# Performance work log

Measured on AMD Instinct MI355X. Metric: run time of the kernel, lower is better.

Reference implementation:

```python
import jax, jax.numpy as jnp
import numpy as np

MUL0, MUL1 = 128, 64
DIM1 = MUL0 + 3 * MUL1          # 320 = dim of 128x0e + 64x1o
DIM2 = 4                        # 1x0e + 1x1o
WDIM, H = 16, 64
# per-instruction weight sizes (mul_in2 = 1), e3nn instruction order
N1 = MUL0 * MUL0                # (0e x 0e -> 0e)
N2 = MUL0 * MUL1                # (0e x 1o -> 1o)
N3 = MUL1 * MUL1                # (1o x 0e -> 1o)
N4 = MUL1 * MUL0                # (1o x 1o -> 0e)
WNUMEL = N1 + N2 + N3 + N4      # 36864
FAN = MUL0 + MUL1               # summed fan-in per output slice = 192
PW0 = float(np.sqrt(1.0 / FAN))         # path weight, component/element norm, l_out=0
PW1 = float(np.sqrt(3.0 / FAN))         # l_out=1 (alpha = 2l+1 = 3)
INV_SQRT3 = float(1.0 / np.sqrt(3.0))   # wigner_3j(1,1,0)/(0,1,1)/(1,0,1) entries
SQRT_K = float(1.0 / np.sqrt(FAN))      # tp_rescale correction (output divided by this)


def setup_inputs() -> dict:
    key = jax.random.key(0)
    ks = jax.random.split(key, 8)
    N = 4096

    def lin(k, fin, fout):
        k1, k2 = jax.random.split(k)
        lim = 1.0 / np.sqrt(fin)
        W = jax.random.uniform(k1, (fin, fout), minval=-lim, maxval=lim, dtype=jnp.float32)
        b = jax.random.uniform(k2, (fout,), minval=-lim, maxval=lim, dtype=jnp.float32)
        return W, b

    W0, b0 = lin(ks[3], WDIM, H)
    W1, b1 = lin(ks[4], H, H)
    W2, b2 = lin(ks[5], H, WNUMEL)
    return {
        "data_in1": jax.random.normal(ks[0], (N, DIM1), dtype=jnp.float32),
        "data_in2": jax.random.normal(ks[1], (N, DIM2), dtype=jnp.float32),
        "weight": jax.random.normal(ks[2], (N, WDIM), dtype=jnp.float32),
        "W0": W0, "b0": b0, "W1": W1, "b1": b1, "W2": W2, "b2": b2,
        "bias": jax.random.uniform(ks[6], (MUL0,), minval=-SQRT_K, maxval=SQRT_K, dtype=jnp.float32),
    }


def _forward(data_in1, data_in2, weight, W0, b0, W1, b1, W2, b2, bias):
    # weight-generating MLP: 16 -> 64 -> 64 -> weight_numel
    h = jax.nn.relu(weight @ W0 + b0)
    h = jax.nn.relu(h @ W1 + b1)
    w = h @ W2 + b2                                   # [N, WNUMEL] per-sample tp weights
    # split inputs into irrep blocks
    s1 = data_in1[:, :MUL0]                           # [N,128]  128x0e
    v1 = data_in1[:, MUL0:].reshape(-1, MUL1, 3)      # [N,64,3]  64x1o
    s2 = data_in2[:, 0]                               # [N]       1x0e
    v2 = data_in2[:, 1:4]                             # [N,3]     1x1o
    # per-instruction weight views (uvw with v=1 collapsed)
    Wa = w[:, :N1].reshape(-1, MUL0, MUL0)                   # 0e x 0e -> 0e
    Wb = w[:, N1:N1 + N2].reshape(-1, MUL0, MUL1)            # 0e x 1o -> 1o
    Wc = w[:, N1 + N2:N1 + N2 + N3].reshape(-1, MUL1, MUL1)  # 1o x 0e -> 1o
    Wd = w[:, N1 + N2 + N3:].reshape(-1, MUL1, MUL0)         # 1o x 1o -> 0e
    dot12 = jnp.einsum('eui,ei->eu', v1, v2)          # [N,64]
    # scalar (0e) output slice: paths Wa (w3j=1) and Wd (w3j = delta/sqrt(3))
    out0 = PW0 * (jnp.einsum('euw,eu->ew', Wa, s1) * s2[:, None]
                  + INV_SQRT3 * jnp.einsum('euw,eu->ew', Wd, dot12))
    # vector (1o) output slice: paths Wb and Wc (w3j = delta/sqrt(3))
    out1 = PW1 * INV_SQRT3 * (
        jnp.einsum('euw,eu->ew', Wb, s1)[:, :, None] * v2[:, None, :]
        + jnp.einsum('euw,eui->ewi', Wc, v1) * s2[:, None, None])
    out = jnp.concatenate([out0, out1.reshape(-1, 3 * MUL1)], axis=1)  # [N,320]
    out = out / SQRT_K                                # tp_rescale: divide by sqrt_k correction
    out = out.at[:, :MUL0].add(bias)                  # bias added on 0e slice only
    return out


def reference(data_in1, data_in2, weight, W0, b0, W1, b1, W2, b2, bias):
    return _forward(data_in1, data_in2, weight, W0, b0, W1, b1, W2, b2, bias)
```

## Files before the change

kernel.cpp:

```cpp
#include <hip/hip_runtime.h>
#include <hip/hip_bf16.h>

typedef __attribute__((ext_vector_type(8))) short short8;
typedef __attribute__((ext_vector_type(4))) float f32x4;

constexpr int N1 = 16384, N2 = 8192, N3 = 4096;
constexpr int WN = 36864;
constexpr float ISQ3 = 0.57735026918962576451f;

__device__ __forceinline__ unsigned short f2bf(float f) {
  unsigned u = __builtin_bit_cast(unsigned, f);
  u += 0x7fffu + ((u >> 16) & 1u);
  return (unsigned short)(u >> 16);
}

#define MFMA(a, b, c) __builtin_amdgcn_mfma_f32_16x16x32_bf16((a), (b), (c), 0, 0, 0)

__global__ __launch_bounds__(256)
void k_prep(const float* __restrict__ wgt, const float* __restrict__ W0,
            const float* __restrict__ b0, const float* __restrict__ W1,
            const float* __restrict__ b1, const float* __restrict__ W2,
            const float* __restrict__ b2, const float* __restrict__ bias,
            const float* __restrict__ d1, const float* __restrict__ d2,
            float* __restrict__ H, unsigned short* __restrict__ Bp,
            float* __restrict__ sAg, float* __restrict__ sBg,
            float* __restrict__ sDg, float* __restrict__ sCg,
            float* __restrict__ d2T, float* __restrict__ out) {
  __shared__ __align__(16) float shm[10400];
  const int bid = blockIdx.x;
  const int tid = threadIdx.x;

  if (bid < 512) {
    float* s1s = shm;
    float* v1s = shm + 1024;
    float* dts = shm + 2560;
    float* s2s = shm + 3072;
    float* v2s = shm + 3080;
    const int e0 = bid * 8;
    for (int x = tid; x < 8 * 320; x += 256) {
      int e = x / 320, c = x % 320;
      float v = d1[(size_t)(e0 + e) * 320 + c];
      if (c < 128) s1s[e * 128 + c] = v;
      else { int q = c - 128; v1s[(e * 64 + q / 3) * 3 + q % 3] = v; }
    }
    if (tid < 32) {
      int e = tid >> 2, c = tid & 3;
      float v = d2[(size_t)(e0 + e) * 4 + c];
      if (c == 0) s2s[e] = v; else v2s[e * 3 + c - 1] = v;
    }
    __syncthreads();
    for (int x = tid; x < 8 * 64; x += 256) {
      int e = x >> 6, u = x & 63;
      dts[e * 64 + u] = v1s[(e * 64 + u) * 3] * v2s[e * 3] +
                        v1s[(e * 64 + u) * 3 + 1] * v2s[e * 3 + 1] +
                        v1s[(e * 64 + u) * 3 + 2] * v2s[e * 3 + 2];
    }
    __syncthreads();
    for (int c = tid; c < 320; c += 256) {
      if (c < 128) {
        const int w = c;
        float ta[8] = {0,0,0,0,0,0,0,0}, td[8] = {0,0,0,0,0,0,0,0};
        for (int u = 0; u < 128; ++u) {
          float bv = b2[u * 128 + w];
#pragma unroll
          for (int e = 0; e < 8; ++e) ta[e] = fmaf(s1s[e * 128 + u], bv, ta[e]);
        }
        for (int u = 0; u < 64; ++u) {
          float bv = b2[N1 + N2 + N3 + u * 128 + w];
#pragma unroll
          for (int e = 0; e < 8; ++e) td[e] = fmaf(dts[e * 64 + u], bv, td[e]);
        }
        const float bw = bias[w];
#pragma unroll
        for (int e = 0; e < 8; ++e)
          out[(size_t)(e0 + e) * 320 + c] = fmaf(s2s[e], ta[e], ISQ3 * td[e]) + bw;
      } else {
        const int q = c - 128, w = q / 3, i = q % 3;
        float tb[8] = {0,0,0,0,0,0,0,0}, tc[8] = {0,0,0,0,0,0,0,0};
        for (int u = 0; u < 128; ++u) {
          float bv = b2[N1 + u * 64 + w];
#pragma unroll
          for (int e = 0; e < 8; ++e) tb[e] = fmaf(s1s[e * 128 + u], bv, tb[e]);
        }
        for (int u = 0; u < 64; ++u) {
          float bv = b2[N1 + N2 + u * 64 + w];
#pragma unroll
          for (int e = 0; e < 8; ++e) tc[e] = fmaf(v1s[(e * 64 + u) * 3 + i], bv, tc[e]);
        }
#pragma unroll
        for (int e = 0; e < 8; ++e)
          out[(size_t)(e0 + e) * 320 + c] = tb[e] * v2s[e * 3 + i] + tc[e] * s2s[e];
      }
    }
  } else if (bid < 1664) {
    const int g = (bid - 512) * 256 + tid;
    const int lane = g & 63;
    const int nth = g >> 6;
    const int kh = nth & 1, nt = nth >> 1;
    const int n = nt * 16 + (lane & 15);
    const int k0 = kh * 32 + (lane >> 4) * 8;
    short8 v;
#pragma unroll
    for (int q = 0; q < 8; ++q) v[q] = (short)f2bf(W2[(size_t)(k0 + q) * WN + n]);
    *(short8*)(Bp + (size_t)g * 8) = v;
  } else if (bid < 2688) {
    float* h0s = shm;
    const int r = tid >> 6, jj = tid & 63;
    const int e = (bid - 1664) * 4 + r;
    float a = b0[jj];
#pragma unroll
    for (int i = 0; i < 16; ++i) a = fmaf(wgt[e * 16 + i], W0[i * 64 + jj], a);
    h0s[r * 64 + jj] = fmaxf(a, 0.f);
    __syncthreads();
    float a1 = b1[jj];
#pragma unroll
    for (int i = 0; i < 64; ++i) a1 = fmaf(h0s[r * 64 + i], W1[i * 64 + jj], a1);
    H[e * 64 + jj] = fmaxf(a1, 0.f);
  } else {
    float* d1s = shm;
    float* d2s = shm + 10272;
    const int e0 = (bid - 2688) * 32;
    for (int x = tid; x < 32 * 320; x += 256) {
      int e = x / 320, c = x % 320;
      d1s[e * 321 + c] = d1[(size_t)(e0 + e) * 320 + c];
    }
    if (tid < 128) d2s[tid] = d2[(size_t)e0 * 4 + tid];
    __syncthreads();
    const int e = tid & 31;
    const float s2 = d2s[e * 4 + 0];
    const float w1 = d2s[e * 4 + 1], w2 = d2s[e * 4 + 2], w3 = d2s[e * 4 + 3];
    for (int row = (tid >> 5); row < 516; row += 8) {
      float v; float* dst;
      if (row < 128)      { v = d1s[e * 321 + row] * s2;            dst = sAg + (size_t)row * 4096; }
      else if (row < 256) { v = d1s[e * 321 + (row - 128)];         dst = sBg + (size_t)(row - 128) * 4096; }
      else if (row < 320) { int u = row - 256;
        v = ISQ3 * (d1s[e * 321 + 128 + 3 * u] * w1 + d1s[e * 321 + 129 + 3 * u] * w2 +
                    d1s[e * 321 + 130 + 3 * u] * w3);               dst = sDg + (size_t)u * 4096; }
      else if (row < 512) { v = d1s[e * 321 + 128 + (row - 320)] * s2; dst = sCg + (size_t)(row - 320) * 4096; }
      else                { v = d2s[e * 4 + (row - 512)];           dst = d2T + (size_t)(row - 512) * 4096; }
      dst[e0 + e] = v;
    }
  }
}

__global__ __launch_bounds__(256, 3)
void k_main(const float* __restrict__ sAg, const float* __restrict__ sBg,
            const float* __restrict__ sDg, const float* __restrict__ sCg,
            const float* __restrict__ d2T, const float* __restrict__ H,
            const unsigned short* __restrict__ Bp, float* __restrict__ out) {
  __shared__ __align__(16) float lds[8704];
  const int bid = blockIdx.x, tid = threadIdx.x;
  const int wid = tid >> 6, lane = tid & 63;
  const int nl = lane & 15, grp = lane >> 4;
  const short8* Bp8 = (const short8*)Bp;
  const f32x4 Z = {0.f, 0.f, 0.f, 0.f};

  if (bid < 512) {
    const int j = bid & 7, tile = bid >> 3, e0 = tile * 64;
    short8 h00, h01, h10, h11, h20, h21, h30, h31;
    {
      const float* hp; short8 v0, v1;
#define LOADH(EF, N0, N1_)                                                     \
      hp = H + (size_t)(e0 + 16 * EF + nl) * 64 + grp * 8;                     \
      _Pragma("unroll") for (int q = 0; q < 8; ++q) {                          \
        v0[q] = (short)f2bf(hp[q]); v1[q] = (short)f2bf(hp[32 + q]); }         \
      N0 = v0; N1_ = v1;
      LOADH(0, h00, h01) LOADH(1, h10, h11) LOADH(2, h20, h21) LOADH(3, h30, h31)
#undef LOADH
    }
    const int uA0 = wid * 32, uD0 = wid * 16;
    const short8* pA = Bp8 + (size_t)(uA0 * 8 + j) * 128 + lane;
    const short8* pD = Bp8 + (size_t)(1792 + uD0 * 8 + j) * 128 + lane;
    const float* qA0 = sAg + (size_t)uA0 * 4096 + e0 + nl;
    const float* qA1 = qA0 + 4096;
    const float* qD  = sDg + (size_t)uD0 * 4096 + e0 + nl;

    short8 A00 = pA[0], A01 = pA[64], A10 = pA[1024], A11 = pA[1088]; pA += 2048;
    short8 D00 = pD[0], D01 = pD[64]; pD += 1024;
    float sa0 = qA0[0], sa1 = qA0[16], sa2 = qA0[32], sa3 = qA0[48];
    float sa4 = qA1[0], sa5 = qA1[16], sa6 = qA1[32], sa7 = qA1[48]; qA0 += 8192; qA1 += 8192;
    float sd0 = qD[0], sd1 = qD[16], sd2 = qD[32], sd3 = qD[48]; qD += 4096;
    short8 B00 = pA[0], B01 = pA[64], B10 = pA[1024], B11 = pA[1088]; pA += 2048;
    short8 E00 = pD[0], E01 = pD[64]; pD += 1024;
    float ta0 = qA0[0], ta1 = qA0[16], ta2 = qA0[32], ta3 = qA0[48];
    float ta4 = qA1[0], ta5 = qA1[16], ta6 = qA1[32], ta7 = qA1[48]; qA0 += 8192; qA1 += 8192;
    float td0 = qD[0], td1 = qD[16], td2 = qD[32], td3 = qD[48]; qD += 4096;

    f32x4 accA[4] = {Z, Z, Z, Z};
    f32x4 accD[4] = {Z, Z, Z, Z};

#define QUAD(P0, P1, S0, S1, S2, S3, AC) do { f32x4 t_;                        \
    t_ = Z; t_ = MFMA(P0, h00, t_); t_ = MFMA(P1, h01, t_); AC[0] += (S0) * t_; \
    t_ = Z; t_ = MFMA(P0, h10, t_); t_ = MFMA(P1, h11, t_); AC[1] += (S1) * t_; \
    t_ = Z; t_ = MFMA(P0, h20, t_); t_ = MFMA(P1, h21, t_); AC[2] += (S2) * t_; \
    t_ = Z; t_ = MFMA(P0, h30, t_); t_ = MFMA(P1, h31, t_); AC[3] += (S3) * t_; } while (0)

#pragma unroll
    for (int t = 0; t < 16; t += 2) {
      QUAD(A00, A01, sa0, sa1, sa2, sa3, accA);
      QUAD(A10, A11, sa4, sa5, sa6, sa7, accA);
      QUAD(D00, D01, sd0, sd1, sd2, sd3, accD);
      if (t < 14) {
        A00 = pA[0]; A01 = pA[64]; A10 = pA[1024]; A11 = pA[1088]; pA += 2048;
        D00 = pD[0]; D01 = pD[64]; pD += 1024;
        sa0 = qA0[0]; sa1 = qA0[16]; sa2 = qA0[32]; sa3 = qA0[48];
        sa4 = qA1[0]; sa5 = qA1[16]; sa6 = qA1[32]; sa7 = qA1[48]; qA0 += 8192; qA1 += 8192;
        sd0 = qD[0]; sd1 = qD[16]; sd2 = qD[32]; sd3 = qD[48]; qD += 4096;
      }
      QUAD(B00, B01, ta0, ta1, ta2, ta3, accA);
      QUAD(B10, B11, ta4, ta5, ta6, ta7, accA);
      QUAD(E00, E01, td0, td1, td2, td3, accD);
      if (t < 13) {
        B00 = pA[0]; B01 = pA[64]; B10 = pA[1024]; B11 = pA[1088]; pA += 2048;
        E00 = pD[0]; E01 = pD[64]; pD += 1024;
        ta0 = qA0[0]; ta1 = qA0[16]; ta2 = qA0[32]; ta3 = qA0[48];
        ta4 = qA1[0]; ta5 = qA1[16]; ta6 = qA1[32]; ta7 = qA1[48]; qA0 += 8192; qA1 += 8192;
        td0 = qD[0]; td1 = qD[16]; td2 = qD[32]; td3 = qD[48]; qD += 4096;
      }
    }
#undef QUAD

#pragma unroll
    for (int eF = 0; eF < 4; ++eF) {
      f32x4 fin = accA[eF] + accD[eF];
      *(f32x4*)&lds[wid * 1280 + (16 * eF + nl) * 20 + grp * 4] = fin;
    }
    __syncthreads();
    {
      const int e = tid >> 2, w4 = (tid & 3) * 4;
      f32x4 s = Z;
#pragma unroll
      for (int wv = 0; wv < 4; ++wv) s += *(const f32x4*)&lds[wv * 1280 + e * 20 + w4];
      f32x4* op = (f32x4*)(out + (size_t)(e0 + e) * 320 + j * 16 + w4);
      *op = *op + s;
    }
  } else {
    const int idx = bid - 512;
    const int j = idx & 3;
    const int tile = ((idx >> 3) << 1) + ((idx >> 2) & 1);
    const int e0 = tile * 32;
    short8 h00, h01, h10, h11;
    {
      const float* hp; short8 v0, v1;
#define LOADH(EF, N0, N1_)                                                     \
      hp = H + (size_t)(e0 + 16 * EF + nl) * 64 + grp * 8;                     \
      _Pragma("unroll") for (int q = 0; q < 8; ++q) {                          \
        v0[q] = (short)f2bf(hp[q]); v1[q] = (short)f2bf(hp[32 + q]); }         \
      N0 = v0; N1_ = v1;
      LOADH(0, h00, h01) LOADH(1, h10, h11)
#undef LOADH
    }
    const int uB0 = wid * 32, uC0 = wid * 16;
    const short8* pB = Bp8 + (size_t)(1024 + uB0 * 4 + j) * 128 + lane;
    const short8* pC = Bp8 + (size_t)(1536 + uC0 * 4 + j) * 128 + lane;
    const float* qB0 = sBg + (size_t)uB0 * 4096 + e0 + nl;
    const float* qB1 = qB0 + 4096;
    const float* qC0 = sCg + (size_t)(uC0 * 3) * 4096 + e0 + nl;
    const float* qC1 = qC0 + 4096;
    const float* qC2 = qC0 + 8192;

    short8 A00 = pB[0], A01 = pB[64], A10 = pB[512], A11 = pB[576]; pB += 1024;
    short8 C00 = pC[0], C01 = pC[64]; pC += 512;
    float sb0 = qB0[0], sb1 = qB0[16], sb2 = qB1[0], sb3 = qB1[16]; qB0 += 8192; qB1 += 8192;
    float sc00 = qC0[0], sc01 = qC0[16], sc10 = qC1[0], sc11 = qC1[16],
          sc20 = qC2[0], sc21 = qC2[16]; qC0 += 12288; qC1 += 12288; qC2 += 12288;
    short8 B00 = pB[0], B01 = pB[64], B10 = pB[512], B11 = pB[576]; pB += 1024;
    short8 E00 = pC[0], E01 = pC[64]; pC += 512;
    float tb0 = qB0[0], tb1 = qB0[16], tb2 = qB1[0], tb3 = qB1[16]; qB0 += 8192; qB1 += 8192;
    float tc00 = qC0[0], tc01 = qC0[16], tc10 = qC1[0], tc11 = qC1[16],
          tc20 = qC2[0], tc21 = qC2[16]; qC0 += 12288; qC1 += 12288; qC2 += 12288;

    f32x4 accB[2] = {Z, Z};
    f32x4 accC0[2] = {Z, Z}, accC1[2] = {Z, Z}, accC2[2] = {Z, Z};

#define DUO(P0, P1, S0, S1) do { f32x4 t_;                                     \
    t_ = Z; t_ = MFMA(P0, h00, t_); t_ = MFMA(P1, h01, t_); accB[0] += (S0) * t_; \
    t_ = Z; t_ = MFMA(P0, h10, t_); t_ = MFMA(P1, h11, t_); accB[1] += (S1) * t_; } while (0)
#define CTRIO(P0, P1, X00, X01, X10, X11, X20, X21) do { f32x4 u0_, u1_;       \
    u0_ = Z; u0_ = MFMA(P0, h00, u0_); u0_ = MFMA(P1, h01, u0_);               \
    u1_ = Z; u1_ = MFMA(P0, h10, u1_); u1_ = MFMA(P1, h11, u1_);               \
    accC0[0] += (X00) * u0_; accC0[1] += (X01) * u1_;                          \
    accC1[0] += (X10) * u0_; accC1[1] += (X11) * u1_;                          \
    accC2[0] += (X20) * u0_; accC2[1] += (X21) * u1_; } while (0)

#pragma unroll
    for (int t = 0; t < 16; t += 2) {
      DUO(A00, A01, sb0, sb1);
      DUO(A10, A11, sb2, sb3);
      CTRIO(C00, C01, sc00, sc01, sc10, sc11, sc20, sc21);
      if (t < 14) {
        A00 = pB[0]; A01 = pB[64]; A10 = pB[512]; A11 = pB[576]; pB += 1024;
        C00 = pC[0]; C01 = pC[64]; pC += 512;
        sb0 = qB0[0]; sb1 = qB0[16]; sb2 = qB1[0]; sb3 = qB1[16]; qB0 += 8192; qB1 += 8192;
        sc00 = qC0[0]; sc01 = qC0[16]; sc10 = qC1[0]; sc11 = qC1[16];
        sc20 = qC2[0]; sc21 = qC2[16]; qC0 += 12288; qC1 += 12288; qC2 += 12288;
      }
      DUO(B00, B01, tb0, tb1);
      DUO(B10, B11, tb2, tb3);
      CTRIO(E00, E01, tc00, tc01, tc10, tc11, tc20, tc21);
      if (t < 13) {
        B00 = pB[0]; B01 = pB[64]; B10 = pB[512]; B11 = pB[576]; pB += 1024;
        E00 = pC[0]; E01 = pC[64]; pC += 512;
        tb0 = qB0[0]; tb1 = qB0[16]; tb2 = qB1[0]; tb3 = qB1[16]; qB0 += 8192; qB1 += 8192;
        tc00 = qC0[0]; tc01 = qC0[16]; tc10 = qC1[0]; tc11 = qC1[16];
        tc20 = qC2[0]; tc21 = qC2[16]; qC0 += 12288; qC1 += 12288; qC2 += 12288;
      }
    }
#undef DUO
#undef CTRIO

#pragma unroll
    for (int eF = 0; eF < 2; ++eF)
#pragma unroll
      for (int r = 0; r < 4; ++r) {
        f32x4 v = {accB[eF][r], accC0[eF][r], accC1[eF][r], accC2[eF][r]};
        *(f32x4*)&lds[wid * 2176 + (16 * eF + nl) * 68 + (grp * 4 + r) * 4] = v;
      }
    __syncthreads();
    for (int p = tid; p < 512; p += 256) {
      const int e = p >> 4, w = p & 15;
      f32x4 s = Z;
#pragma unroll
      for (int wv = 0; wv < 4; ++wv) s += *(const f32x4*)&lds[wv * 2176 + e * 68 + w * 4];
      const float v20 = d2T[4096 + e0 + e], v21 = d2T[8192 + e0 + e], v22 = d2T[12288 + e0 + e];
      float* op = out + (size_t)(e0 + e) * 320 + 128 + (size_t)(j * 16 + w) * 3;
      op[0] += s[0] * v20 + s[1];
      op[1] += s[0] * v21 + s[2];
      op[2] += s[0] * v22 + s[3];
    }
  }
}

extern "C" void kernel_launch(void* const* d_in, const int* in_sizes, int n_in,
                              void* d_out, int out_size, void* d_ws, size_t ws_size,
                              hipStream_t stream) {
  const float* d1   = (const float*)d_in[0];
  const float* d2   = (const float*)d_in[1];
  const float* wgt  = (const float*)d_in[2];
  const float* W0   = (const float*)d_in[3];
  const float* b0   = (const float*)d_in[4];
  const float* W1   = (const float*)d_in[5];
  const float* b1   = (const float*)d_in[6];
  const float* W2   = (const float*)d_in[7];
  const float* b2   = (const float*)d_in[8];
  const float* bias = (const float*)d_in[9];
  float* out = (float*)d_out;

  char* ws = (char*)d_ws;
  float* H           = (float*)(ws);
  unsigned short* Bp = (unsigned short*)(ws + (1u << 20));
  float* sAg         = (float*)(ws + (6u << 20));
  float* sBg         = (float*)(ws + (8u << 20));
  float* sDg         = (float*)(ws + (10u << 20));
  float* sCg         = (float*)(ws + (11u << 20));
  float* d2T         = (float*)(ws + (14u << 20));

  k_prep<<<2816, 256, 0, stream>>>(wgt, W0, b0, W1, b1, W2, b2, bias, d1, d2,
                                   H, Bp, sAg, sBg, sDg, sCg, d2T, out);
  k_main<<<1024, 256, 0, stream>>>(sAg, sBg, sDg, sCg, d2T, H, Bp, out);
}
```

Before: 73.86 us.

## Split main kernel into A/B and D/C kernels with scaled-H MFMA operands

Replaces the single k_main with two kernels. k_ab pairs the A and B paths, which both contract against s1. It folds the per-sample s1 scalar into the H operand before the MFMA, scaling H by s1 and packing to bf16, and applies s2 or v2 afterwards, so the sAg staging array and its prep writes go away. k_dc handles the D and C paths. Both kernels use 512-thread blocks with an XCD-aware block-to-tile mapping, packed bf16 conversion via v_cvt_pk_bf16_f32, and a two-stage LDS reduction across waves. The change adds a second launch and extra VALU conversion work per u iteration, and it does read-modify-write on out from two kernels.

New measurement: 79.29 us. +7.3%, slower.

```diff
diff --git a/kernel.cpp b/kernel.cpp
--- a/kernel.cpp
+++ b/kernel.cpp
@@ -3,6 +3,8 @@
 
 typedef __attribute__((ext_vector_type(8))) short short8;
 typedef __attribute__((ext_vector_type(4))) float f32x4;
+typedef __attribute__((ext_vector_type(2))) float f32x2;
+typedef __attribute__((ext_vector_type(4))) unsigned uint4v;
 
 constexpr int N1 = 16384, N2 = 8192, N3 = 4096;
 constexpr int WN = 36864;
@@ -14,7 +16,30 @@
   return (unsigned short)(u >> 16);
 }
 
+__device__ __forceinline__ unsigned pkbf(float a, float b) {
+  unsigned r;
+  asm("v_cvt_pk_bf16_f32 %0, %1, %2" : "=v"(r) : "v"(a), "v"(b));
+  return r;
+}
+
 #define MFMA(a, b, c) __builtin_amdgcn_mfma_f32_16x16x32_bf16((a), (b), (c), 0, 0, 0)
+
+#define SYNTH2(S, HA, G0, G1) do {                                            \
+    f32x2 sv_; sv_[0] = (S); sv_[1] = (S);                                    \
+    uint4v w0_, w1_;                                                          \
+    f32x2 p0_ = sv_ * HA[0], p1_ = sv_ * HA[1], p2_ = sv_ * HA[2], p3_ = sv_ * HA[3]; \
+    w0_[0] = pkbf(p0_[0], p0_[1]); w0_[1] = pkbf(p1_[0], p1_[1]);             \
+    w0_[2] = pkbf(p2_[0], p2_[1]); w0_[3] = pkbf(p3_[0], p3_[1]);             \
+    f32x2 p4_ = sv_ * HA[4], p5_ = sv_ * HA[5], p6_ = sv_ * HA[6], p7_ = sv_ * HA[7]; \
+    w1_[0] = pkbf(p4_[0], p4_[1]); w1_[1] = pkbf(p5_[0], p5_[1]);             \
+    w1_[2] = pkbf(p6_[0], p6_[1]); w1_[3] = pkbf(p7_[0], p7_[1]);             \
+    G0 = __builtin_bit_cast(short8, w0_); G1 = __builtin_bit_cast(short8, w1_); \
+  } while (0)
+
+#define CVT8(X0, X1, G) do { uint4v w_;                                       \
+    w_[0] = pkbf(X0[0], X0[1]); w_[1] = pkbf(X0[2], X0[3]);                   \
+    w_[2] = pkbf(X1[0], X1[1]); w_[3] = pkbf(X1[2], X1[3]);                   \
+    G = __builtin_bit_cast(short8, w_); } while (0)
 
 __global__ __launch_bounds__(256)
 void k_prep(const float* __restrict__ wgt, const float* __restrict__ W0,
@@ -23,9 +48,9 @@
             const float* __restrict__ b2, const float* __restrict__ bias,
             const float* __restrict__ d1, const float* __restrict__ d2,
             float* __restrict__ H, unsigned short* __restrict__ Bp,
-            float* __restrict__ sAg, float* __restrict__ sBg,
-            float* __restrict__ sDg, float* __restrict__ sCg,
-            float* __restrict__ d2T, float* __restrict__ out) {
+            float* __restrict__ sBg, float* __restrict__ sDg,
+            float* __restrict__ sCg, float* __restrict__ d2T,
+            float* __restrict__ out) {
   __shared__ __align__(16) float shm[10400];
   const int bid = blockIdx.x;
   const int tid = threadIdx.x;
@@ -129,10 +154,9 @@
     const int e = tid & 31;
     const float s2 = d2s[e * 4 + 0];
     const float w1 = d2s[e * 4 + 1], w2 = d2s[e * 4 + 2], w3 = d2s[e * 4 + 3];
-    for (int row = (tid >> 5); row < 516; row += 8) {
+    for (int row = 128 + (tid >> 5); row < 516; row += 8) {
       float v; float* dst;
-      if (row < 128)      { v = d1s[e * 321 + row] * s2;            dst = sAg + (size_t)row * 4096; }
-      else if (row < 256) { v = d1s[e * 321 + (row - 128)];         dst = sBg + (size_t)(row - 128) * 4096; }
+      if (row < 256)      { v = d1s[e * 321 + (row - 128)];         dst = sBg + (size_t)(row - 128) * 4096; }
       else if (row < 320) { int u = row - 256;
         v = ISQ3 * (d1s[e * 321 + 128 + 3 * u] * w1 + d1s[e * 321 + 129 + 3 * u] * w2 +
                     d1s[e * 321 + 130 + 3 * u] * w3);               dst = sDg + (size_t)u * 4096; }
@@ -143,190 +167,213 @@
   }
 }
 
-__global__ __launch_bounds__(256, 3)
-void k_main(const float* __restrict__ sAg, const float* __restrict__ sBg,
-            const float* __restrict__ sDg, const float* __restrict__ sCg,
-            const float* __restrict__ d2T, const float* __restrict__ H,
-            const unsigned short* __restrict__ Bp, float* __restrict__ out) {
-  __shared__ __align__(16) float lds[8704];
-  const int bid = blockIdx.x, tid = threadIdx.x;
+__global__ __launch_bounds__(512, 2)
+void k_ab(const float* __restrict__ sBg, const float* __restrict__ d2T,
+          const float* __restrict__ H, const unsigned short* __restrict__ Bp,
+          float* __restrict__ out) {
+  __shared__ float buf[4][32][49];
+  const int tid = threadIdx.x;
   const int wid = tid >> 6, lane = tid & 63;
   const int nl = lane & 15, grp = lane >> 4;
+  const int xcd = blockIdx.x & 7;
+  const int jq = xcd & 3;
+  const int et = (int)(blockIdx.x >> 3) | ((xcd >> 2) << 6);
+  const int e0 = et * 32;
   const short8* Bp8 = (const short8*)Bp;
-  const f32x4 Z = {0.f, 0.f, 0.f, 0.f};
-
-  if (bid < 512) {
-    const int j = bid & 7, tile = bid >> 3, e0 = tile * 64;
-    short8 h00, h01, h10, h11, h20, h21, h30, h31;
-    {
-      const float* hp; short8 v0, v1;
-#define LOADH(EF, N0, N1_)                                                     \
-      hp = H + (size_t)(e0 + 16 * EF + nl) * 64 + grp * 8;                     \
-      _Pragma("unroll") for (int q = 0; q < 8; ++q) {                          \
-        v0[q] = (short)f2bf(hp[q]); v1[q] = (short)f2bf(hp[32 + q]); }         \
-      N0 = v0; N1_ = v1;
-      LOADH(0, h00, h01) LOADH(1, h10, h11) LOADH(2, h20, h21) LOADH(3, h30, h31)
-#undef LOADH
-    }
-    const int uA0 = wid * 32, uD0 = wid * 16;
-    const short8* pA = Bp8 + (size_t)(uA0 * 8 + j) * 128 + lane;
-    const short8* pD = Bp8 + (size_t)(1792 + uD0 * 8 + j) * 128 + lane;
-    const float* qA0 = sAg + (size_t)uA0 * 4096 + e0 + nl;
-    const float* qA1 = qA0 + 4096;
-    const float* qD  = sDg + (size_t)uD0 * 4096 + e0 + nl;
-
-    short8 A00 = pA[0], A01 = pA[64], A10 = pA[1024], A11 = pA[1088]; pA += 2048;
-    short8 D00 = pD[0], D01 = pD[64]; pD += 1024;
-    float sa0 = qA0[0], sa1 = qA0[16], sa2 = qA0[32], sa3 = qA0[48];
-    float sa4 = qA1[0], sa5 = qA1[16], sa6 = qA1[32], sa7 = qA1[48]; qA0 += 8192; qA1 += 8192;
-    float sd0 = qD[0], sd1 = qD[16], sd2 = qD[32], sd3 = qD[48]; qD += 4096;
-    short8 B00 = pA[0], B01 = pA[64], B10 = pA[1024], B11 = pA[1088]; pA += 2048;
-    short8 E00 = pD[0], E01 = pD[64]; pD += 1024;
-    float ta0 = qA0[0], ta1 = qA0[16], ta2 = qA0[32], ta3 = qA0[48];
-    float ta4 = qA1[0], ta5 = qA1[16], ta6 = qA1[32], ta7 = qA1[48]; qA0 += 8192; qA1 += 8192;
-    float td0 = qD[0], td1 = qD[16], td2 = qD[32], td3 = qD[48]; qD += 4096;
-
-    f32x4 accA[4] = {Z, Z, Z, Z};
-    f32x4 accD[4] = {Z, Z, Z, Z};
-
-#define QUAD(P0, P1, S0, S1, S2, S3, AC) do { f32x4 t_;                        \
-    t_ = Z; t_ = MFMA(P0, h00, t_); t_ = MFMA(P1, h01, t_); AC[0] += (S0) * t_; \
-    t_ = Z; t_ = MFMA(P0, h10, t_); t_ = MFMA(P1, h11, t_); AC[1] += (S1) * t_; \
-    t_ = Z; t_ = MFMA(P0, h20, t_); t_ = MFMA(P1, h21, t_); AC[2] += (S2) * t_; \
-    t_ = Z; t_ = MFMA(P0, h30, t_); t_ = MFMA(P1, h31, t_); AC[3] += (S3) * t_; } while (0)
-
-#pragma unroll
-    for (int t = 0; t < 16; t += 2) {
-      QUAD(A00, A01, sa0, sa1, sa2, sa3, accA);
-      QUAD(A10, A11, sa4, sa5, sa6, sa7, accA);
-      QUAD(D00, D01, sd0, sd1, sd2, sd3, accD);
-      if (t < 14) {
-        A00 = pA[0]; A01 = pA[64]; A10 = pA[1024]; A11 = pA[1088]; pA += 2048;
-        D00 = pD[0]; D01 = pD[64]; pD += 1024;
-        sa0 = qA0[0]; sa1 = qA0[16]; sa2 = qA0[32]; sa3 = qA0[48];
-        sa4 = qA1[0]; sa5 = qA1[16]; sa6 = qA1[32]; sa7 = qA1[48]; qA0 += 8192; qA1 += 8192;
-        sd0 = qD[0]; sd1 = qD[16]; sd2 = qD[32]; sd3 = qD[48]; qD += 4096;
-      }
-      QUAD(B00, B01, ta0, ta1, ta2, ta3, accA);
-      QUAD(B10, B11, ta4, ta5, ta6, ta7, accA);
-      QUAD(E00, E01, td0, td1, td2, td3, accD);
-      if (t < 13) {
-        B00 = pA[0]; B01 = pA[64]; B10 = pA[1024]; B11 = pA[1088]; pA += 2048;
-        E00 = pD[0]; E01 = pD[64]; pD += 1024;
-        ta0 = qA0[0]; ta1 = qA0[16]; ta2 = qA0[32]; ta3 = qA0[48];
-        ta4 = qA1[0]; ta5 = qA1[16]; ta6 = qA1[32]; ta7 = qA1[48]; qA0 += 8192; qA1 += 8192;
-        td0 = qD[0]; td1 = qD[16]; td2 = qD[32]; td3 = qD[48]; qD += 4096;
-      }
-    }
-#undef QUAD
-
-#pragma unroll
-    for (int eF = 0; eF < 4; ++eF) {
-      f32x4 fin = accA[eF] + accD[eF];
-      *(f32x4*)&lds[wid * 1280 + (16 * eF + nl) * 20 + grp * 4] = fin;
-    }
-    __syncthreads();
-    {
-      const int e = tid >> 2, w4 = (tid & 3) * 4;
-      f32x4 s = Z;
-#pragma unroll
-      for (int wv = 0; wv < 4; ++wv) s += *(const f32x4*)&lds[wv * 1280 + e * 20 + w4];
-      f32x4* op = (f32x4*)(out + (size_t)(e0 + e) * 320 + j * 16 + w4);
-      *op = *op + s;
-    }
-  } else {
-    const int idx = bid - 512;
-    const int j = idx & 3;
-    const int tile = ((idx >> 3) << 1) + ((idx >> 2) & 1);
-    const int e0 = tile * 32;
-    short8 h00, h01, h10, h11;
-    {
-      const float* hp; short8 v0, v1;
-#define LOADH(EF, N0, N1_)                                                     \
-      hp = H + (size_t)(e0 + 16 * EF + nl) * 64 + grp * 8;                     \
-      _Pragma("unroll") for (int q = 0; q < 8; ++q) {                          \
-        v0[q] = (short)f2bf(hp[q]); v1[q] = (short)f2bf(hp[32 + q]); }         \
-      N0 = v0; N1_ = v1;
-      LOADH(0, h00, h01) LOADH(1, h10, h11)
-#undef LOADH
-    }
-    const int uB0 = wid * 32, uC0 = wid * 16;
-    const short8* pB = Bp8 + (size_t)(1024 + uB0 * 4 + j) * 128 + lane;
-    const short8* pC = Bp8 + (size_t)(1536 + uC0 * 4 + j) * 128 + lane;
-    const float* qB0 = sBg + (size_t)uB0 * 4096 + e0 + nl;
-    const float* qB1 = qB0 + 4096;
-    const float* qC0 = sCg + (size_t)(uC0 * 3) * 4096 + e0 + nl;
-    const float* qC1 = qC0 + 4096;
-    const float* qC2 = qC0 + 8192;
-
-    short8 A00 = pB[0], A01 = pB[64], A10 = pB[512], A11 = pB[576]; pB += 1024;
-    short8 C00 = pC[0], C01 = pC[64]; pC += 512;
-    float sb0 = qB0[0], sb1 = qB0[16], sb2 = qB1[0], sb3 = qB1[16]; qB0 += 8192; qB1 += 8192;
-    float sc00 = qC0[0], sc01 = qC0[16], sc10 = qC1[0], sc11 = qC1[16],
-          sc20 = qC2[0], sc21 = qC2[16]; qC0 += 12288; qC1 += 12288; qC2 += 12288;
-    short8 B00 = pB[0], B01 = pB[64], B10 = pB[512], B11 = pB[576]; pB += 1024;
-    short8 E00 = pC[0], E01 = pC[64]; pC += 512;
-    float tb0 = qB0[0], tb1 = qB0[16], tb2 = qB1[0], tb3 = qB1[16]; qB0 += 8192; qB1 += 8192;
-    float tc00 = qC0[0], tc01 = qC0[16], tc10 = qC1[0], tc11 = qC1[16],
-          tc20 = qC2[0], tc21 = qC2[16]; qC0 += 12288; qC1 += 12288; qC2 += 12288;
-
-    f32x4 accB[2] = {Z, Z};
-    f32x4 accC0[2] = {Z, Z}, accC1[2] = {Z, Z}, accC2[2] = {Z, Z};
-
-#define DUO(P0, P1, S0, S1) do { f32x4 t_;                                     \
-    t_ = Z; t_ = MFMA(P0, h00, t_); t_ = MFMA(P1, h01, t_); accB[0] += (S0) * t_; \
-    t_ = Z; t_ = MFMA(P0, h10, t_); t_ = MFMA(P1, h11, t_); accB[1] += (S1) * t_; } while (0)
-#define CTRIO(P0, P1, X00, X01, X10, X11, X20, X21) do { f32x4 u0_, u1_;       \
-    u0_ = Z; u0_ = MFMA(P0, h00, u0_); u0_ = MFMA(P1, h01, u0_);               \
-    u1_ = Z; u1_ = MFMA(P0, h10, u1_); u1_ = MFMA(P1, h11, u1_);               \
-    accC0[0] += (X00) * u0_; accC0[1] += (X01) * u1_;                          \
-    accC1[0] += (X10) * u0_; accC1[1] += (X11) * u1_;                          \
-    accC2[0] += (X20) * u0_; accC2[1] += (X21) * u1_; } while (0)
-
-#pragma unroll
-    for (int t = 0; t < 16; t += 2) {
-      DUO(A00, A01, sb0, sb1);
-      DUO(A10, A11, sb2, sb3);
-      CTRIO(C00, C01, sc00, sc01, sc10, sc11, sc20, sc21);
-      if (t < 14) {
-        A00 = pB[0]; A01 = pB[64]; A10 = pB[512]; A11 = pB[576]; pB += 1024;
-        C00 = pC[0]; C01 = pC[64]; pC += 512;
-        sb0 = qB0[0]; sb1 = qB0[16]; sb2 = qB1[0]; sb3 = qB1[16]; qB0 += 8192; qB1 += 8192;
-        sc00 = qC0[0]; sc01 = qC0[16]; sc10 = qC1[0]; sc11 = qC1[16];
-        sc20 = qC2[0]; sc21 = qC2[16]; qC0 += 12288; qC1 += 12288; qC2 += 12288;
-      }
-      DUO(B00, B01, tb0, tb1);
-      DUO(B10, B11, tb2, tb3);
-      CTRIO(E00, E01, tc00, tc01, tc10, tc11, tc20, tc21);
-      if (t < 13) {
-        B00 = pB[0]; B01 = pB[64]; B10 = pB[512]; B11 = pB[576]; pB += 1024;
-        E00 = pC[0]; E01 = pC[64]; pC += 512;
-        tb0 = qB0[0]; tb1 = qB0[16]; tb2 = qB1[0]; tb3 = qB1[16]; qB0 += 8192; qB1 += 8192;
-        tc00 = qC0[0]; tc01 = qC0[16]; tc10 = qC1[0]; tc11 = qC1[16];
-        tc20 = qC2[0]; tc21 = qC2[16]; qC0 += 12288; qC1 += 12288; qC2 += 12288;
-      }
-    }
-#undef DUO
-#undef CTRIO
-
-#pragma unroll
-    for (int eF = 0; eF < 2; ++eF)
-#pragma unroll
-      for (int r = 0; r < 4; ++r) {
-        f32x4 v = {accB[eF][r], accC0[eF][r], accC1[eF][r], accC2[eF][r]};
-        *(f32x4*)&lds[wid * 2176 + (16 * eF + nl) * 68 + (grp * 4 + r) * 4] = v;
-      }
-    __syncthreads();
-    for (int p = tid; p < 512; p += 256) {
-      const int e = p >> 4, w = p & 15;
-      f32x4 s = Z;
-#pragma unroll
-      for (int wv = 0; wv < 4; ++wv) s += *(const f32x4*)&lds[wv * 2176 + e * 68 + w * 4];
-      const float v20 = d2T[4096 + e0 + e], v21 = d2T[8192 + e0 + e], v22 = d2T[12288 + e0 + e];
-      float* op = out + (size_t)(e0 + e) * 320 + 128 + (size_t)(j * 16 + w) * 3;
-      op[0] += s[0] * v20 + s[1];
-      op[1] += s[0] * v21 + s[2];
-      op[2] += s[0] * v22 + s[3];
+  const f32x4 Zv = {0.f, 0.f, 0.f, 0.f};
+
+  f32x2 hf0[8], hf1[8];
+  {
+    const float* hp0 = H + (size_t)(e0 + nl) * 64 + grp * 8;
+    const float* hp1 = H + (size_t)(e0 + 16 + nl) * 64 + grp * 8;
+    f32x4 x0 = *(const f32x4*)(hp0),      x1 = *(const f32x4*)(hp0 + 4);
+    f32x4 x2 = *(const f32x4*)(hp0 + 32), x3 = *(const f32x4*)(hp0 + 36);
+    f32x4 y0 = *(const f32x4*)(hp1),      y1 = *(const f32x4*)(hp1 + 4);
+    f32x4 y2 = *(const f32x4*)(hp1 + 32), y3 = *(const f32x4*)(hp1 + 36);
+    hf0[0][0]=x0[0]; hf0[0][1]=x0[1]; hf0[1][0]=x0[2]; hf0[1][1]=x0[3];
+    hf0[2][0]=x1[0]; hf0[2][1]=x1[1]; hf0[3][0]=x1[2]; hf0[3][1]=x1[3];
+    hf0[4][0]=x2[0]; hf0[4][1]=x2[1]; hf0[5][0]=x2[2]; hf0[5][1]=x2[3];
+    hf0[6][0]=x3[0]; hf0[6][1]=x3[1]; hf0[7][0]=x3[2]; hf0[7][1]=x3[3];
+    hf1[0][0]=y0[0]; hf1[0][1]=y0[1]; hf1[1][0]=y0[2]; hf1[1][1]=y0[3];
+    hf1[2][0]=y1[0]; hf1[2][1]=y1[1]; hf1[3][0]=y1[2]; hf1[3][1]=y1[3];
+    hf1[4][0]=y2[0]; hf1[4][1]=y2[1]; hf1[5][0]=y2[2]; hf1[5][1]=y2[3];
+    hf1[6][0]=y3[0]; hf1[6][1]=y3[1]; hf1[7][0]=y3[2]; hf1[7][1]=y3[3];
+  }
+
+  f32x4 accA00 = Zv, accA01 = Zv, accA10 = Zv, accA11 = Zv;
+  f32x4 accB0 = Zv, accB1 = Zv;
+
+  const int u0 = wid * 16;
+  const short8* pa = Bp8 + ((size_t)u0 * 8 + jq * 2) * 128 + lane;
+  const short8* pb = Bp8 + ((size_t)(1024 + u0 * 4 + jq)) * 128 + lane;
+  const float* sb0 = sBg + (size_t)u0 * 4096 + e0 + nl;
+  const float* sb1 = sb0 + 16;
+
+#pragma unroll 4
+  for (int ul = 0; ul < 16; ++ul) {
+    short8 F00 = pa[0], F01 = pa[64], F10 = pa[128], F11 = pa[192];
+    short8 G0 = pb[0], G1 = pb[64];
+    float s0 = sb0[0], s1v = sb1[0];
+    pa += 1024; pb += 512; sb0 += 4096; sb1 += 4096;
+    short8 g00, g01, g10, g11;
+    SYNTH2(s0, hf0, g00, g01);
+    SYNTH2(s1v, hf1, g10, g11);
+    accA00 = MFMA(F01, g01, MFMA(F00, g00, accA00));
+    accA01 = MFMA(F01, g11, MFMA(F00, g10, accA01));
+    accA10 = MFMA(F11, g01, MFMA(F10, g00, accA10));
+    accA11 = MFMA(F11, g11, MFMA(F10, g10, accA11));
+    accB0  = MFMA(G1,  g01, MFMA(G0,  g00, accB0));
+    accB1  = MFMA(G1,  g11, MFMA(G0,  g10, accB1));
+  }
+
+  const int s = wid & 3;
+  if (wid >= 4) {
+#pragma unroll
+    for (int r = 0; r < 4; ++r) {
+      buf[s][nl][grp * 4 + r]           = accA00[r];
+      buf[s][nl][16 + grp * 4 + r]      = accA10[r];
+      buf[s][16 + nl][grp * 4 + r]      = accA01[r];
+      buf[s][16 + nl][16 + grp * 4 + r] = accA11[r];
+      buf[s][nl][32 + grp * 4 + r]      = accB0[r];
+      buf[s][16 + nl][32 + grp * 4 + r] = accB1[r];
+    }
+  }
+  __syncthreads();
+  if (wid < 4) {
+#pragma unroll
+    for (int r = 0; r < 4; ++r) {
+      buf[s][nl][grp * 4 + r]           += accA00[r];
+      buf[s][nl][16 + grp * 4 + r]      += accA10[r];
+      buf[s][16 + nl][grp * 4 + r]      += accA01[r];
+      buf[s][16 + nl][16 + grp * 4 + r] += accA11[r];
+      buf[s][nl][32 + grp * 4 + r]      += accB0[r];
+      buf[s][16 + nl][32 + grp * 4 + r] += accB1[r];
+    }
+  }
+  __syncthreads();
+#pragma unroll
+  for (int it = 0; it < 3; ++it) {
+    const int p = tid + it * 512;
+    const int e = p / 48, c = p % 48;
+    float v = buf[0][e][c] + buf[1][e][c] + buf[2][e][c] + buf[3][e][c];
+    float* orow = out + (size_t)(e0 + e) * 320;
+    if (c < 32) {
+      orow[jq * 32 + c] += d2T[e0 + e] * v;
+    } else {
+      const int q = c - 32;
+      float* op = orow + 128 + (size_t)(jq * 16 + q) * 3;
+      op[0] += v * d2T[4096 + e0 + e];
+      op[1] += v * d2T[8192 + e0 + e];
+      op[2] += v * d2T[12288 + e0 + e];
+    }
+  }
+}
+
+__global__ __launch_bounds__(512, 2)
+void k_dc(const float* __restrict__ sDg, const float* __restrict__ sCg,
+          const float* __restrict__ H, const unsigned short* __restrict__ Bp,
+          float* __restrict__ out) {
+  __shared__ float buf[4][32][81];
+  const int tid = threadIdx.x;
+  const int wid = tid >> 6, lane = tid & 63;
+  const int nl = lane & 15, grp = lane >> 4;
+  const int xcd = blockIdx.x & 7;
+  const int jq = xcd & 3;
+  const int et = (int)(blockIdx.x >> 3) | ((xcd >> 2) << 6);
+  const int e0 = et * 32;
+  const short8* Bp8 = (const short8*)Bp;
+  const f32x4 Zv = {0.f, 0.f, 0.f, 0.f};
+
+  short8 hb00, hb01, hb10, hb11;
+  {
+    const float* hp0 = H + (size_t)(e0 + nl) * 64 + grp * 8;
+    const float* hp1 = H + (size_t)(e0 + 16 + nl) * 64 + grp * 8;
+    f32x4 x0 = *(const f32x4*)(hp0),      x1 = *(const f32x4*)(hp0 + 4);
+    f32x4 x2 = *(const f32x4*)(hp0 + 32), x3 = *(const f32x4*)(hp0 + 36);
+    f32x4 y0 = *(const f32x4*)(hp1),      y1 = *(const f32x4*)(hp1 + 4);
+    f32x4 y2 = *(const f32x4*)(hp1 + 32), y3 = *(const f32x4*)(hp1 + 36);
+    CVT8(x0, x1, hb00); CVT8(x2, x3, hb01);
+    CVT8(y0, y1, hb10); CVT8(y2, y3, hb11);
+  }
+
+  f32x4 accD00 = Zv, accD01 = Zv, accD10 = Zv, accD11 = Zv;
+  f32x4 accC00 = Zv, accC01 = Zv, accC02 = Zv;
+  f32x4 accC10 = Zv, accC11 = Zv, accC12 = Zv;
+
+  const int u0 = wid * 8;
+  const short8* pd = Bp8 + ((size_t)(1792 + u0 * 8 + jq * 2)) * 128 + lane;
+  const short8* pc = Bp8 + ((size_t)(1536 + u0 * 4 + jq)) * 128 + lane;
+  const float* sd0 = sDg + (size_t)u0 * 4096 + e0 + nl;
+  const float* sc0 = sCg + (size_t)(3 * u0) * 4096 + e0 + nl;
+
+#pragma unroll 4
+  for (int ul = 0; ul < 8; ++ul) {
+    short8 FD00 = pd[0], FD01 = pd[64], FD10 = pd[128], FD11 = pd[192];
+    short8 FC0 = pc[0], FC1 = pc[64];
+    float sdE = sd0[0], sdO = sd0[16];
+    float sc00 = sc0[0],          sc01 = sc0[16];
+    float sc10 = sc0[4096],       sc11 = sc0[4096 + 16];
+    float sc20 = sc0[8192],       sc21 = sc0[8192 + 16];
+    pd += 1024; pc += 512; sd0 += 4096; sc0 += 12288;
+    f32x4 t00 = MFMA(FD01, hb01, MFMA(FD00, hb00, Zv));
+    f32x4 t01 = MFMA(FD01, hb11, MFMA(FD00, hb10, Zv));
+    f32x4 t10 = MFMA(FD11, hb01, MFMA(FD10, hb00, Zv));
+    f32x4 t11 = MFMA(FD11, hb11, MFMA(FD10, hb10, Zv));
+    accD00 += sdE * t00; accD01 += sdO * t01;
+    accD10 += sdE * t10; accD11 += sdO * t11;
+    f32x4 tc0 = MFMA(FC1, hb01, MFMA(FC0, hb00, Zv));
+    f32x4 tc1 = MFMA(FC1, hb11, MFMA(FC0, hb10, Zv));
+    accC00 += sc00 * tc0; accC01 += sc10 * tc0; accC02 += sc20 * tc0;
+    accC10 += sc01 * tc1; accC11 += sc11 * tc1; accC12 += sc21 * tc1;
+  }
+
+  const int s = wid & 3;
+  if (wid >= 4) {
+#pragma unroll
+    for (int r = 0; r < 4; ++r) {
+      buf[s][nl][grp * 4 + r]           = accD00[r];
+      buf[s][nl][16 + grp * 4 + r]      = accD10[r];
+      buf[s][16 + nl][grp * 4 + r]      = accD01[r];
+      buf[s][16 + nl][16 + grp * 4 + r] = accD11[r];
+      const int cb = 32 + (grp * 4 + r) * 3;
+      buf[s][nl][cb]          = accC00[r];
+      buf[s][nl][cb + 1]      = accC01[r];
+      buf[s][nl][cb + 2]      = accC02[r];
+      buf[s][16 + nl][cb]     = accC10[r];
+      buf[s][16 + nl][cb + 1] = accC11[r];
+      buf[s][16 + nl][cb + 2] = accC12[r];
+    }
+  }
+  __syncthreads();
+  if (wid < 4) {
+#pragma unroll
+    for (int r = 0; r < 4; ++r) {
+      buf[s][nl][grp * 4 + r]           += accD00[r];
+      buf[s][nl][16 + grp * 4 + r]      += accD10[r];
+      buf[s][16 + nl][grp * 4 + r]      += accD01[r];
+      buf[s][16 + nl][16 + grp * 4 + r] += accD11[r];
+      const int cb = 32 + (grp * 4 + r) * 3;
+      buf[s][nl][cb]          += accC00[r];
+      buf[s][nl][cb + 1]      += accC01[r];
+      buf[s][nl][cb + 2]      += accC02[r];
+      buf[s][16 + nl][cb]     += accC10[r];
+      buf[s][16 + nl][cb + 1] += accC11[r];
+      buf[s][16 + nl][cb + 2] += accC12[r];
+    }
+  }
+  __syncthreads();
+#pragma unroll
+  for (int it = 0; it < 5; ++it) {
+    const int p = tid + it * 512;
+    const int e = p / 80, c = p % 80;
+    float v = buf[0][e][c] + buf[1][e][c] + buf[2][e][c] + buf[3][e][c];
+    float* orow = out + (size_t)(e0 + e) * 320;
+    if (c < 32) {
+      orow[jq * 32 + c] += v;
+    } else {
+      const int q = c - 32;
+      const int w1l = q / 3, i = q - w1l * 3;
+      orow[128 + (size_t)(jq * 16 + w1l) * 3 + i] += v;
     }
   }
 }
@@ -349,13 +396,13 @@
   char* ws = (char*)d_ws;
   float* H           = (float*)(ws);
   unsigned short* Bp = (unsigned short*)(ws + (1u << 20));
-  float* sAg         = (float*)(ws + (6u << 20));
   float* sBg         = (float*)(ws + (8u << 20));
   float* sDg         = (float*)(ws + (10u << 20));
   float* sCg         = (float*)(ws + (11u << 20));
   float* d2T         = (float*)(ws + (14u << 20));
 
   k_prep<<<2816, 256, 0, stream>>>(wgt, W0, b0, W1, b1, W2, b2, bias, d1, d2,
-                                   H, Bp, sAg, sBg, sDg, sCg, d2T, out);
-  k_main<<<1024, 256, 0, stream>>>(sAg, sBg, sDg, sCg, d2T, H, Bp, out);
-}
+                                   H, Bp, sBg, sDg, sCg, d2T, out);
+  k_ab<<<512, 512, 0, stream>>>(sBg, d2T, H, Bp, out);
+  k_dc<<<512, 512, 0, stream>>>(sDg, sCg, H, Bp, out);
+}
```
